# Performance work log

Measured on AMD Instinct MI355X. Metric: run time of the kernel, lower is better.

## Reference

```python
import jax, jax.numpy as jnp
import numpy as np

N, E, FE, H, G, L, OUT = 50000, 300000, 64, 256, 256, 4, 128
BN_EPS = 1e-5


def setup_inputs() -> dict:
    key = jax.random.key(0)
    ks = jax.random.split(key, 12)
    s = 0.05
    return dict(
        x=jax.random.normal(ks[0], (N, H), jnp.float32),
        edge_index=jax.random.randint(ks[1], (2, E), 0, N, dtype=jnp.int64),
        edge_attr=jax.random.normal(ks[2], (E, FE), jnp.float32),
        batch=jnp.sort(jax.random.randint(ks[3], (N,), 0, G, dtype=jnp.int64)),
        bond_W1=jax.random.normal(ks[4], (L, FE, H), jnp.float32) * s,
        bond_b1=jnp.zeros((L, H), jnp.float32),
        bond_W2=jax.random.normal(ks[5], (L, H, H), jnp.float32) * s,
        bond_b2=jnp.zeros((L, H), jnp.float32),
        mlp_W1=jax.random.normal(ks[6], (L, H, H), jnp.float32) * s,
        mlp_b1=jnp.zeros((L, H), jnp.float32),
        mlp_W2=jax.random.normal(ks[7], (L, H, H), jnp.float32) * s,
        mlp_b2=jnp.zeros((L, H), jnp.float32),
        eps=jnp.zeros((L,), jnp.float32),
        bn_gamma=jnp.ones((L, H), jnp.float32),
        bn_beta=jnp.zeros((L, H), jnp.float32),
        fc1_W=jax.random.normal(ks[8], (L * H, H), jnp.float32) * s,
        fc1_b=jnp.zeros((H,), jnp.float32),
        fc4_W=jax.random.normal(ks[9], (H, OUT), jnp.float32) * s,
        fc4_b=jnp.zeros((OUT,), jnp.float32),
    )


def reference(x, edge_index, edge_attr, batch,
              bond_W1, bond_b1, bond_W2, bond_b2,
              mlp_W1, mlp_b1, mlp_W2, mlp_b2,
              eps, bn_gamma, bn_beta,
              fc1_W, fc1_b, fc4_W, fc4_b):
    src, dst = edge_index[0], edge_index[1]  # x_j gathered from src, scatter-add to dst
    x_lst = []
    for l in range(L):
        # bond encoder: Linear -> ReLU -> Linear on edge features [E, FE] -> [E, H]
        e = jax.nn.relu(edge_attr @ bond_W1[l] + bond_b1[l]) @ bond_W2[l] + bond_b2[l]
        # message = relu(x_j + e), aggregate = scatter-add over destination nodes
        msg = jax.nn.relu(x[src] + e)  # [E, H]
        aggr = jax.ops.segment_sum(msg, dst, num_segments=N)  # [N, H]
        h = (1.0 + eps[l]) * x + aggr
        h = jax.nn.relu(h @ mlp_W1[l] + mlp_b1[l]) @ mlp_W2[l] + mlp_b2[l]
        h = jax.nn.relu(h)
        # BatchNorm over the node dimension (training-style batch statistics)
        mu = jnp.mean(h, axis=0)
        var = jnp.var(h, axis=0)
        x = (h - mu) * jax.lax.rsqrt(var + BN_EPS) * bn_gamma[l] + bn_beta[l]
        x_lst.append(x)
    xc = jnp.concatenate(x_lst, axis=-1)  # [N, L*H]
    # global mean pool over graphs
    sums = jax.ops.segment_sum(xc, batch, num_segments=G)  # [G, L*H]
    cnts = jax.ops.segment_sum(jnp.ones((N,), xc.dtype), batch, num_segments=G)
    pooled = sums / jnp.maximum(cnts, 1.0)[:, None]
    h = jax.nn.relu(pooled @ fc1_W + fc1_b)
    # dropout p=0.5 in eval mode -> identity
    return h @ fc4_W + fc4_b  # [G, OUT]
```

## Files before the change

kernel.cpp:

```cpp
#include <hip/hip_runtime.h>

#define NN 50000
#define NE 300000
#define FEA 64
#define HD 256
#define NG 256
#define NL 4
#define OD 128
#define SCB ((NN + 255) / 256)

typedef unsigned short u16;
typedef unsigned int u32;
typedef __attribute__((ext_vector_type(8))) short short8;
typedef __attribute__((ext_vector_type(4))) float f32x4;

__device__ __forceinline__ u16 f2h(float f) {
    union { _Float16 h; u16 u; } v; v.h = (_Float16)f; return v.u;
}
__device__ __forceinline__ float h2f(u16 u) {
    union { u16 u; _Float16 h; } v; v.u = u; return (float)v.h;
}

typedef const __attribute__((address_space(1))) unsigned int gas_u32;
typedef __attribute__((address_space(3))) unsigned int las_u32;
__device__ __forceinline__ void gld16(const void* g, void* l) {
    __builtin_amdgcn_global_load_lds((gas_u32*)g, (las_u32*)l, 16, 0, 0);
}

__global__ __launch_bounds__(256, 2) void edge_k(
    const u16* __restrict__ eattrS, const u16* __restrict__ W1t,
    const float* __restrict__ bb1, const u16* __restrict__ W2t,
    const float* __restrict__ bb2,
    const int* __restrict__ srcI, const int* __restrict__ dstI,
    const u16* __restrict__ xh, float* __restrict__ aggr)
{
    __shared__ __align__(16) u16 bufW[256 * 64];
    __shared__ __align__(16) u16 bufT[64 * 256];
    __shared__ int dstL[64];
    __shared__ int srcL[64];
    const int tid = threadIdx.x;
    const int lane = tid & 63;
    const int w = tid >> 6;
    const int q = lane >> 4, c15 = lane & 15;
    const int e0 = blockIdx.x * 64;
    const int wb = tid & ~63;

    if (tid < 64) {
        int er = e0 + tid;
        int erc = er < NE ? er : NE - 1;
        dstL[tid] = (er < NE) ? dstI[erc] : -1;
        srcL[tid] = srcI[erc];
    }
#pragma unroll
    for (int it = 0; it < 2; ++it) {
        const int i = it * 256 + tid;
        const int m = i >> 3, kb = i & 7;
        int row = e0 + m; if (row > NE - 1) row = NE - 1;
        gld16(eattrS + (size_t)row * FEA + ((kb ^ (m & 7)) * 8),
              &bufT[(it * 256 + wb) * 8]);
    }
#pragma unroll
    for (int it = 0; it < 8; ++it) {
        const int i = it * 256 + tid;
        const int n = i >> 3, kb = i & 7;
        gld16(W1t + (size_t)n * FEA + ((kb ^ (n & 7)) * 8),
              &bufW[(it * 256 + wb) * 8]);
    }
    __syncthreads();

    f32x4 acc1[4][4];
#pragma unroll
    for (int i = 0; i < 4; ++i)
#pragma unroll
        for (int j = 0; j < 4; ++j) acc1[i][j] = (f32x4)0.0f;
#pragma unroll
    for (int s = 0; s < 2; ++s) {
        short8 af[4], bf[4];
#pragma unroll
        for (int t = 0; t < 4; ++t) {
            const int kga = s * 4 + q;
            const int mm = t * 16 + c15;
            af[t] = *(const short8*)&bufT[mm * 64 + ((kga ^ (mm & 7)) * 8)];
            const int nn = w * 64 + t * 16 + c15;
            bf[t] = *(const short8*)&bufW[nn * 64 + ((kga ^ (nn & 7)) * 8)];
        }
        __builtin_amdgcn_s_setprio(1);
#pragma unroll
        for (int tm = 0; tm < 4; ++tm)
#pragma unroll
            for (int tn = 0; tn < 4; ++tn)
                acc1[tm][tn] = __builtin_amdgcn_mfma_f32_16x16x32_f16(
                    af[tm], bf[tn], acc1[tm][tn], 0, 0, 0);
        __builtin_amdgcn_s_setprio(0);
    }
    __syncthreads();

    auto stageW2 = [&](int cc) {
        const int k0c = cc * 32;
        const int hB = (cc & 1) * 1024;
#pragma unroll
        for (int it = 0; it < 4; ++it) {
            const int i = it * 256 + tid;
            const int n = i >> 2, j = i & 3;
            gld16(W2t + (size_t)n * HD + k0c + ((j ^ ((n >> 1) & 3)) * 8),
                  &bufW[(hB + it * 256 + wb) * 8]);
        }
    };
    stageW2(0);

    {
        float b1f[4];
#pragma unroll
        for (int tn = 0; tn < 4; ++tn)
            b1f[tn] = bb1[w * 64 + tn * 16 + c15];
#pragma unroll
        for (int tm = 0; tm < 4; ++tm)
#pragma unroll
            for (int tn = 0; tn < 4; ++tn) {
                const int col = w * 64 + tn * 16 + c15;
                const int kb = col >> 3;
#pragma unroll
                for (int r = 0; r < 4; ++r) {
                    const int row = tm * 16 + q * 4 + r;
                    float v = acc1[tm][tn][r] + b1f[tn];
                    v = v > 0.0f ? v : 0.0f;
                    bufT[row * 256 + ((kb ^ (row & 7)) * 8) + (col & 7)] = f2h(v);
                }
            }
    }
    __syncthreads();

    f32x4 acc2[4][4];
#pragma unroll
    for (int i = 0; i < 4; ++i)
#pragma unroll
        for (int j = 0; j < 4; ++j) acc2[i][j] = (f32x4)0.0f;
#pragma unroll
    for (int c = 0; c < 8; ++c) {
        if (c < 7) {
            stageW2(c + 1);
        } else {
#pragma unroll
            for (int it = 0; it < 4; ++it) {
                const int i = it * 256 + tid;
                const int row = i >> 5, ch = i & 31;
                gld16(xh + (size_t)srcL[row] * HD + ch * 8,
                      &bufW[(it * 256 + wb) * 8]);
            }
        }
        short8 af[4], bf[4];
        const u16* hp = &bufW[(c & 1) * 8192];
#pragma unroll
        for (int t = 0; t < 4; ++t) {
            const int mm = t * 16 + c15;
            const int kbg = c * 4 + q;
            af[t] = *(const short8*)&bufT[mm * 256 + ((kbg ^ (mm & 7)) * 8)];
            const int nn = w * 64 + t * 16 + c15;
            bf[t] = *(const short8*)&hp[nn * 32 + ((q ^ ((nn >> 1) & 3)) * 8)];
        }
        __builtin_amdgcn_s_setprio(1);
#pragma unroll
        for (int tm = 0; tm < 4; ++tm)
#pragma unroll
            for (int tn = 0; tn < 4; ++tn)
                acc2[tm][tn] = __builtin_amdgcn_mfma_f32_16x16x32_f16(
                    af[tm], bf[tn], acc2[tm][tn], 0, 0, 0);
        __builtin_amdgcn_s_setprio(0);
        __syncthreads();
    }

#pragma unroll
    for (int it = 0; it < 4; ++it) {
        const int i = 1024 + it * 256 + tid;
        const int row = i >> 5, ch = i & 31;
        gld16(xh + (size_t)srcL[row] * HD + ch * 8,
              &bufW[(1024 + it * 256 + wb) * 8]);
    }
    float b2f[4];
#pragma unroll
    for (int tn = 0; tn < 4; ++tn)
        b2f[tn] = bb2[w * 64 + tn * 16 + c15];
    __syncthreads();

#pragma unroll
    for (int tm = 0; tm < 4; ++tm)
#pragma unroll
        for (int r = 0; r < 4; ++r) {
            const int row = tm * 16 + q * 4 + r;
            if (e0 + row < NE) {
#pragma unroll
                for (int tn = 0; tn < 4; ++tn) {
                    const int col = w * 64 + tn * 16 + c15;
                    float v = acc2[tm][tn][r] + b2f[tn]
                            + h2f(bufW[row * 256 + col]);
                    v = v > 0.0f ? v : 0.0f;
                    bufT[row * 256 + col] = f2h(v);
                }
            }
        }
    __syncthreads();

    {
        const int hiR = (NE - e0 < 64) ? (NE - e0) : 64;
        float s = 0.0f;
        int cur = dstL[0];
        for (int rI = 0; rI < hiR; ++rI) {
            const int d = dstL[rI];
            if (d != cur) {
                if (s != 0.0f) unsafeAtomicAdd(&aggr[(size_t)cur * HD + tid], s);
                cur = d; s = 0.0f;
            }
            s += h2f(bufT[rI * 256 + tid]);
        }
        if (cur >= 0 && s != 0.0f)
            unsafeAtomicAdd(&aggr[(size_t)cur * HD + tid], s);
    }
}

__global__ __launch_bounds__(256, 2) void node_k(
    const u16* __restrict__ xh, const float* __restrict__ aggr,
    const float* __restrict__ epsv, int l,
    const u16* __restrict__ M1t, const float* __restrict__ mb1,
    const u16* __restrict__ M2t, const float* __restrict__ mb2,
    u16* __restrict__ hb, float* __restrict__ bns, float* __restrict__ bnq)
{
    __shared__ __align__(16) u16 bufW[256 * 64];
    __shared__ __align__(16) u16 bufT[64 * 256];
    const int tid = threadIdx.x;
    const int lane = tid & 63;
    const int w = tid >> 6;
    const int q = lane >> 4, c15 = lane & 15;
    const int n0b = blockIdx.x * 64;
    const float e1 = 1.0f + epsv[l];
    const int wb = tid & ~63;

    auto stageM = [&](const u16* Mt, int cc) {
        const int k0c = cc * 32;
        const int hB = (cc & 1) * 1024;
#pragma unroll
        for (int it = 0; it < 4; ++it) {
            const int i = it * 256 + tid;
            const int n = i >> 2, j = i & 3;
            gld16(Mt + (size_t)n * HD + k0c + ((j ^ ((n >> 1) & 3)) * 8),
                  &bufW[(hB + it * 256 + wb) * 8]);
        }
    };
    stageM(M1t, 0);

#pragma unroll
    for (int it = 0; it < 8; ++it) {
        const int i = it * 256 + tid;
        const int m = i >> 5, kb = i & 31;
        int row = n0b + m; if (row > NN - 1) row = NN - 1;
        const size_t base = (size_t)row * HD + kb * 8;
        short8 xv = *(const short8*)(xh + base);
        float4 a0 = *(const float4*)(aggr + base);
        float4 a1 = *(const float4*)(aggr + base + 4);
        u16 o[8];
        o[0] = f2h(e1 * h2f((u16)xv[0]) + a0.x);
        o[1] = f2h(e1 * h2f((u16)xv[1]) + a0.y);
        o[2] = f2h(e1 * h2f((u16)xv[2]) + a0.z);
        o[3] = f2h(e1 * h2f((u16)xv[3]) + a0.w);
        o[4] = f2h(e1 * h2f((u16)xv[4]) + a1.x);
        o[5] = f2h(e1 * h2f((u16)xv[5]) + a1.y);
        o[6] = f2h(e1 * h2f((u16)xv[6]) + a1.z);
        o[7] = f2h(e1 * h2f((u16)xv[7]) + a1.w);
        *(short8*)&bufT[m * 256 + ((kb ^ (m & 7)) * 8)] = *(short8*)o;
    }
    __syncthreads();

    f32x4 acc1[4][4];
#pragma unroll
    for (int i = 0; i < 4; ++i)
#pragma unroll
        for (int j = 0; j < 4; ++j) acc1[i][j] = (f32x4)0.0f;
#pragma unroll
    for (int c = 0; c < 8; ++c) {
        if (c < 7) stageM(M1t, c + 1);
        else       stageM(M2t, 0);
        short8 af[4], bf[4];
        const u16* hp = &bufW[(c & 1) * 8192];
#pragma unroll
        for (int t = 0; t < 4; ++t) {
            const int mm = t * 16 + c15;
            const int kbg = c * 4 + q;
            af[t] = *(const short8*)&bufT[mm * 256 + ((kbg ^ (mm & 7)) * 8)];
            const int nn = w * 64 + t * 16 + c15;
            bf[t] = *(const short8*)&hp[nn * 32 + ((q ^ ((nn >> 1) & 3)) * 8)];
        }
        __builtin_amdgcn_s_setprio(1);
#pragma unroll
        for (int tm = 0; tm < 4; ++tm)
#pragma unroll
            for (int tn = 0; tn < 4; ++tn)
                acc1[tm][tn] = __builtin_amdgcn_mfma_f32_16x16x32_f16(
                    af[tm], bf[tn], acc1[tm][tn], 0, 0, 0);
        __builtin_amdgcn_s_setprio(0);
        __syncthreads();
    }

    {
        float b1f[4];
#pragma unroll
        for (int tn = 0; tn < 4; ++tn)
            b1f[tn] = mb1[w * 64 + tn * 16 + c15];
#pragma unroll
        for (int tm = 0; tm < 4; ++tm)
#pragma unroll
            for (int tn = 0; tn < 4; ++tn) {
                const int col = w * 64 + tn * 16 + c15;
                const int kb = col >> 3;
#pragma unroll
                for (int r = 0; r < 4; ++r) {
                    const int row = tm * 16 + q * 4 + r;
                    float v = acc1[tm][tn][r] + b1f[tn];
                    v = v > 0.0f ? v : 0.0f;
                    bufT[row * 256 + ((kb ^ (row & 7)) * 8) + (col & 7)] = f2h(v);
                }
            }
    }
    __syncthreads();

    f32x4 acc2[4][4];
#pragma unroll
    for (int i = 0; i < 4; ++i)
#pragma unroll
        for (int j = 0; j < 4; ++j) acc2[i][j] = (f32x4)0.0f;
#pragma unroll
    for (int c = 0; c < 8; ++c) {
        if (c < 7) stageM(M2t, c + 1);
        short8 af[4], bf[4];
        const u16* hp = &bufW[(c & 1) * 8192];
#pragma unroll
        for (int t = 0; t < 4; ++t) {
            const int mm = t * 16 + c15;
            const int kbg = c * 4 + q;
            af[t] = *(const short8*)&bufT[mm * 256 + ((kbg ^ (mm & 7)) * 8)];
            const int nn = w * 64 + t * 16 + c15;
            bf[t] = *(const short8*)&hp[nn * 32 + ((q ^ ((nn >> 1) & 3)) * 8)];
        }
        __builtin_amdgcn_s_setprio(1);
#pragma unroll
        for (int tm = 0; tm < 4; ++tm)
#pragma unroll
            for (int tn = 0; tn < 4; ++tn)
                acc2[tm][tn] = __builtin_amdgcn_mfma_f32_16x16x32_f16(
                    af[tm], bf[tn], acc2[tm][tn], 0, 0, 0);
        __builtin_amdgcn_s_setprio(0);
        __syncthreads();
    }

    float b2f[4];
#pragma unroll
    for (int tn = 0; tn < 4; ++tn)
        b2f[tn] = mb2[w * 64 + tn * 16 + c15];
    float ps[4] = {0, 0, 0, 0}, pq[4] = {0, 0, 0, 0};
#pragma unroll
    for (int tm = 0; tm < 4; ++tm) {
#pragma unroll
        for (int r = 0; r < 4; ++r) {
            const int grow = n0b + tm * 16 + q * 4 + r;
            if (grow < NN) {
#pragma unroll
                for (int tn = 0; tn < 4; ++tn) {
                    const int col = w * 64 + tn * 16 + c15;
                    float v = acc2[tm][tn][r] + b2f[tn];
                    v = v > 0.0f ? v : 0.0f;
                    hb[(size_t)grow * HD + col] = f2h(v);
                    ps[tn] += v; pq[tn] += v * v;
                }
            }
        }
    }
#pragma unroll
    for (int tn = 0; tn < 4; ++tn) {
        float s = ps[tn], sq = pq[tn];
        s += __shfl_down(s, 32, 64);  sq += __shfl_down(sq, 32, 64);
        s += __shfl_down(s, 16, 64);  sq += __shfl_down(sq, 16, 64);
        if (q == 0) {
            const int col = w * 64 + tn * 16 + c15;
            unsafeAtomicAdd(&bns[col], s);
            unsafeAtomicAdd(&bnq[col], sq);
        }
    }
}


__global__ void transpose_k(const float* __restrict__ in, u16* __restrict__ oh,
                            int Kw, int Nw) {
    int i = blockIdx.x * blockDim.x + threadIdx.x;
    int tot = NL * Kw * Nw;
    if (i < tot) {
        int l = i / (Kw * Nw), rem = i % (Kw * Nw);
        int k = rem / Nw, n = rem % Nw;
        oh[(size_t)l * Kw * Nw + (size_t)n * Kw + k] = f2h(in[i]);
    }
}

__global__ void cvt_k(const float* __restrict__ in, u16* __restrict__ outh, int tot) {
    int i = blockIdx.x * blockDim.x + threadIdx.x;
    if (i < tot) outh[i] = f2h(in[i]);
}

__global__ void egather_k(const float* __restrict__ eattr, const int* __restrict__ perm,
                          u16* __restrict__ eattrS) {
    int i = blockIdx.x * blockDim.x + threadIdx.x;
    if (i < NE * FEA) {
        int row = i >> 6, k = i & 63;
        eattrS[i] = f2h(eattr[(size_t)perm[row] * FEA + k]);
    }
}

__global__ void zero_layer_k(float* __restrict__ aggr, float* __restrict__ bns,
                             float* __restrict__ bnq) {
    int i = blockIdx.x * blockDim.x + threadIdx.x;
    if (i < NN * HD) aggr[i] = 0.0f;
    if (i < HD) { bns[i] = 0.0f; bnq[i] = 0.0f; }
}

__global__ void zerof_k(float* __restrict__ p, int n) {
    int i = blockIdx.x * blockDim.x + threadIdx.x;
    if (i < n) p[i] = 0.0f;
}

__global__ void bnfin_k(const float* __restrict__ bns, const float* __restrict__ bnq,
                        const float* __restrict__ gamma, const float* __restrict__ beta,
                        int l, float* __restrict__ ab) {
    int c = threadIdx.x;
    float mu = bns[c] * (1.0f / (float)NN);
    float var = bnq[c] * (1.0f / (float)NN) - mu * mu;
    if (var < 0.0f) var = 0.0f;
    float a = gamma[l * HD + c] * rsqrtf(var + 1e-5f);
    float b = beta[l * HD + c] - mu * a;
    ab[c] = a; ab[HD + c] = b;
}

__global__ void bnapply_k(const u16* __restrict__ hb, const float* __restrict__ ab,
                          const int* __restrict__ batch, u16* __restrict__ xh,
                          float* __restrict__ pooled, int l) {
    const int t = threadIdx.x;
    const int n0 = blockIdx.x * 64;
    const float a = ab[t], b = ab[HD + t];
    const int hi = (NN - n0 < 64) ? (NN - n0) : 64;
    float s = 0.0f;
    int cur = batch[n0];
    for (int r = 0; r < hi; ++r) {
        const size_t idx = (size_t)(n0 + r) * HD + t;
        float v = a * h2f(hb[idx]) + b;
        xh[idx] = f2h(v);
        const int g = batch[n0 + r];
        if (g != cur) {
            unsafeAtomicAdd(&pooled[(size_t)cur * (NL * HD) + l * HD + t], s);
            s = 0.0f; cur = g;
        }
        s += v;
    }
    unsafeAtomicAdd(&pooled[(size_t)cur * (NL * HD) + l * HD + t], s);
}


__global__ void zeroi_k(int* __restrict__ a, int n) {
    int i = blockIdx.x * blockDim.x + threadIdx.x;
    if (i < n) a[i] = 0;
}

__global__ void hist_k(const int* __restrict__ dst, int* __restrict__ hist) {
    int e = blockIdx.x * blockDim.x + threadIdx.x;
    if (e < NE) atomicAdd(&hist[dst[e]], 1);
}

__global__ void sumblk_k(const int* __restrict__ hist, int* __restrict__ psum) {
    __shared__ int red[256];
    int b = blockIdx.x, t = threadIdx.x, i = b * 256 + t;
    red[t] = (i < NN) ? hist[i] : 0;
    __syncthreads();
    for (int o = 128; o > 0; o >>= 1) {
        if (t < o) red[t] += red[t + o];
        __syncthreads();
    }
    if (t == 0) psum[b] = red[0];
}

__global__ void scanblk_k(int* __restrict__ psum) {
    __shared__ int sc[256];
    int t = threadIdx.x;
    int v = (t < SCB) ? psum[t] : 0;
    sc[t] = v; __syncthreads();
    for (int o = 1; o < 256; o <<= 1) {
        int x = (t >= o) ? sc[t - o] : 0;
        __syncthreads(); sc[t] += x; __syncthreads();
    }
    if (t < SCB) psum[t] = sc[t] - v;
}

__global__ void scanfin_k(const int* __restrict__ hist, const int* __restrict__ psum,
                          int* __restrict__ rowptr) {
    __shared__ int sc[256];
    int b = blockIdx.x, t = threadIdx.x, i = b * 256 + t;
    int v = (i < NN) ? hist[i] : 0;
    sc[t] = v; __syncthreads();
    for (int o = 1; o < 256; o <<= 1) {
        int x = (t >= o) ? sc[t - o] : 0;
        __syncthreads(); sc[t] += x; __syncthreads();
    }
    if (i < NN) rowptr[i] = psum[b] + sc[t] - v;
    if (i == NN - 1) rowptr[NN] = psum[b] + sc[t];
}

__global__ void copyi_k(const int* __restrict__ src, int* __restrict__ dst, int n) {
    int i = blockIdx.x * blockDim.x + threadIdx.x;
    if (i < n) dst[i] = src[i];
}

__global__ void scatter_k(const int* __restrict__ dst, int* __restrict__ next,
                          int* __restrict__ perm) {
    int e = blockIdx.x * blockDim.x + threadIdx.x;
    if (e < NE) {
        int p = atomicAdd(&next[dst[e]], 1);
        perm[p] = e;
    }
}

__global__ void permsd_k(const int* __restrict__ eidx, const int* __restrict__ perm,
                         int* __restrict__ srcS, int* __restrict__ dstS) {
    int i = blockIdx.x * blockDim.x + threadIdx.x;
    if (i < NE) {
        int e = perm[i];
        srcS[i] = eidx[e];
        dstS[i] = eidx[NE + e];
    }
}


__global__ void zcnt_k(int* __restrict__ cnts) {
    if (threadIdx.x < NG) cnts[threadIdx.x] = 0;
}

__global__ void count_k(const int* __restrict__ batch, int* __restrict__ cnts) {
    int i = blockIdx.x * blockDim.x + threadIdx.x;
    if (i < NN) atomicAdd(&cnts[batch[i]], 1);
}

__global__ void fc_k(const float* __restrict__ pooled, const int* __restrict__ cnts,
                     const float* __restrict__ W1, const float* __restrict__ b1,
                     const float* __restrict__ W4, const float* __restrict__ b4,
                     float* __restrict__ out) {
    __shared__ float pl[NL * HD];
    __shared__ float hm[HD];
    int g = blockIdx.x, t = threadIdx.x;
    const float inv = 1.0f / fmaxf((float)cnts[g], 1.0f);
#pragma unroll
    for (int j = 0; j < 4; ++j)
        pl[t + j * 256] = pooled[(size_t)g * 1024 + t + j * 256] * inv;
    __syncthreads();
    float a = b1[t];
    for (int k = 0; k < 1024; ++k) a += pl[k] * W1[k * 256 + t];
    hm[t] = a > 0.0f ? a : 0.0f;
    __syncthreads();
    if (t < OD) {
        float o = b4[t];
        for (int k = 0; k < 256; ++k) o += hm[k] * W4[k * OD + t];
        out[g * OD + t] = o;
    }
}


extern "C" void kernel_launch(void* const* d_in, const int* in_sizes, int n_in,
                              void* d_out, int out_size, void* d_ws, size_t ws_size,
                              hipStream_t stream) {
    const float* x_in  = (const float*)d_in[0];
    const int*   eidx  = (const int*)d_in[1];
    const float* eattr = (const float*)d_in[2];
    const int*   batch = (const int*)d_in[3];
    const float* bW1   = (const float*)d_in[4];
    const float* bb1   = (const float*)d_in[5];
    const float* bW2   = (const float*)d_in[6];
    const float* bb2   = (const float*)d_in[7];
    const float* mW1   = (const float*)d_in[8];
    const float* mb1   = (const float*)d_in[9];
    const float* mW2   = (const float*)d_in[10];
    const float* mb2   = (const float*)d_in[11];
    const float* epsv  = (const float*)d_in[12];
    const float* gamma = (const float*)d_in[13];
    const float* beta  = (const float*)d_in[14];
    const float* fc1W  = (const float*)d_in[15];
    const float* fc1b  = (const float*)d_in[16];
    const float* fc4W  = (const float*)d_in[17];
    const float* fc4b  = (const float*)d_in[18];
    float* out = (float*)d_out;
    (void)in_sizes; (void)n_in; (void)out_size; (void)ws_size;

    size_t off = 0;
    auto alloc = [&](size_t bytes) -> char* {
        char* r = (char*)d_ws + off;
        off = (off + bytes + 255) & ~(size_t)255;
        return r;
    };
    u16*   xh   = (u16*)alloc((size_t)NN * HD * 2);
    float* aggr = (float*)alloc((size_t)NN * HD * 4);
    u16*   hb   = (u16*)alloc((size_t)NN * HD * 2);
    u16*   eattrS = (u16*)alloc((size_t)NE * FEA * 2);
    u16*   W1t  = (u16*)alloc((size_t)NL * FEA * HD * 2);
    u16*   W2t  = (u16*)alloc((size_t)NL * HD * HD * 2);
    u16*   M1t  = (u16*)alloc((size_t)NL * HD * HD * 2);
    u16*   M2t  = (u16*)alloc((size_t)NL * HD * HD * 2);
    float* bns  = (float*)alloc(HD * 4);
    float* bnq  = (float*)alloc(HD * 4);
    float* ab   = (float*)alloc(2 * HD * 4);
    int*   cnts = (int*)alloc(NG * 4);
    float* pooled = (float*)alloc((size_t)NG * NL * HD * 4);
    int*   hist  = (int*)alloc((size_t)NN * 4);
    int*   psum  = (int*)alloc((size_t)SCB * 4);
    int*   rowptr = (int*)alloc((size_t)(NN + 1) * 4);
    int*   perm  = (int*)alloc((size_t)NE * 4);
    int*   srcS  = (int*)alloc((size_t)NE * 4);
    int*   dstS  = (int*)alloc((size_t)NE * 4);

    const int NEL = NN * HD;
    const int EB = (NEL + 255) / 256;
    const int NEB = (NE + 255) / 256;

    transpose_k<<<(NL * FEA * HD + 255) / 256, 256, 0, stream>>>(bW1, W1t, FEA, HD);
    transpose_k<<<(NL * HD * HD + 255) / 256, 256, 0, stream>>>(bW2, W2t, HD, HD);
    transpose_k<<<(NL * HD * HD + 255) / 256, 256, 0, stream>>>(mW1, M1t, HD, HD);
    transpose_k<<<(NL * HD * HD + 255) / 256, 256, 0, stream>>>(mW2, M2t, HD, HD);

    cvt_k<<<EB, 256, 0, stream>>>(x_in, xh, NEL);

    zeroi_k<<<(NN + 255) / 256, 256, 0, stream>>>(hist, NN);
    hist_k<<<NEB, 256, 0, stream>>>(eidx + NE, hist);
    sumblk_k<<<SCB, 256, 0, stream>>>(hist, psum);
    scanblk_k<<<1, 256, 0, stream>>>(psum);
    scanfin_k<<<SCB, 256, 0, stream>>>(hist, psum, rowptr);
    copyi_k<<<(NN + 255) / 256, 256, 0, stream>>>(rowptr, hist, NN);
    scatter_k<<<NEB, 256, 0, stream>>>(eidx + NE, hist, perm);
    permsd_k<<<NEB, 256, 0, stream>>>(eidx, perm, srcS, dstS);
    egather_k<<<(NE * FEA + 255) / 256, 256, 0, stream>>>(eattr, perm, eattrS);

    zcnt_k<<<1, 256, 0, stream>>>(cnts);
    count_k<<<(NN + 255) / 256, 256, 0, stream>>>(batch, cnts);
    zerof_k<<<(NG * NL * HD + 255) / 256, 256, 0, stream>>>(pooled, NG * NL * HD);

    const int EGB = (NE + 63) / 64;
    const int NGB = (NN + 63) / 64;

    for (int l = 0; l < NL; ++l) {
        zero_layer_k<<<EB, 256, 0, stream>>>(aggr, bns, bnq);
        edge_k<<<EGB, 256, 0, stream>>>(
            eattrS, W1t + (size_t)l * FEA * HD, bb1 + l * HD,
            W2t + (size_t)l * HD * HD, bb2 + l * HD,
            srcS, dstS, xh, aggr);
        node_k<<<NGB, 256, 0, stream>>>(
            xh, aggr, epsv, l,
            M1t + (size_t)l * HD * HD, mb1 + l * HD,
            M2t + (size_t)l * HD * HD, mb2 + l * HD,
            hb, bns, bnq);
        bnfin_k<<<1, HD, 0, stream>>>(bns, bnq, gamma, beta, l, ab);
        bnapply_k<<<NGB, 256, 0, stream>>>(hb, ab, batch, xh, pooled, l);
    }
    fc_k<<<NG, 256, 0, stream>>>(pooled, cnts, fc1W, fc1b, fc4W, fc4b, out);
}
```

Baseline: 1.342 ms.

## Transpose MFMA outputs for vectorized LDS stores and column-wise segment reduction

Swaps the MFMA A/B operands in the first GEMM of the edge and node kernels so each lane holds four consecutive output features. The bias-ReLU epilogue can then write 8-byte packed fp16 vectors into the swizzled LDS tile instead of scalar 2-byte stores. The edge kernel's final message tile is stored transposed, so the scatter-add loop reads 16-byte vectors per feature column rather than one fp16 per row. Destination indices are now read directly from global memory inside the reduction loop instead of being staged in shared memory, which adds repeated scalar global loads of dstI.

```diff
diff --git a/kernel.cpp b/kernel.cpp
--- a/kernel.cpp
+++ b/kernel.cpp
@@ -12,6 +12,7 @@
 typedef unsigned short u16;
 typedef unsigned int u32;
 typedef __attribute__((ext_vector_type(8))) short short8;
+typedef __attribute__((ext_vector_type(4))) short s16x4;
 typedef __attribute__((ext_vector_type(4))) float f32x4;
 
 __device__ __forceinline__ u16 f2h(float f) {
@@ -36,7 +37,6 @@
 {
     __shared__ __align__(16) u16 bufW[256 * 64];
     __shared__ __align__(16) u16 bufT[64 * 256];
-    __shared__ int dstL[64];
     __shared__ int srcL[64];
     const int tid = threadIdx.x;
     const int lane = tid & 63;
@@ -48,7 +48,6 @@
     if (tid < 64) {
         int er = e0 + tid;
         int erc = er < NE ? er : NE - 1;
-        dstL[tid] = (er < NE) ? dstI[erc] : -1;
         srcL[tid] = srcI[erc];
     }
 #pragma unroll
@@ -90,7 +89,7 @@
 #pragma unroll
             for (int tn = 0; tn < 4; ++tn)
                 acc1[tm][tn] = __builtin_amdgcn_mfma_f32_16x16x32_f16(
-                    af[tm], bf[tn], acc1[tm][tn], 0, 0, 0);
+                    bf[tm], af[tn], acc1[tm][tn], 0, 0, 0);
         __builtin_amdgcn_s_setprio(0);
     }
     __syncthreads();
@@ -109,24 +108,24 @@
     stageW2(0);
 
     {
-        float b1f[4];
-#pragma unroll
-        for (int tn = 0; tn < 4; ++tn)
-            b1f[tn] = bb1[w * 64 + tn * 16 + c15];
-#pragma unroll
-        for (int tm = 0; tm < 4; ++tm)
+#pragma unroll
+        for (int tm = 0; tm < 4; ++tm) {
+            const float4 b1v = *(const float4*)(bb1 + w * 64 + tm * 16 + q * 4);
+            const int kb = w * 8 + tm * 2 + (q >> 1);
 #pragma unroll
             for (int tn = 0; tn < 4; ++tn) {
-                const int col = w * 64 + tn * 16 + c15;
-                const int kb = col >> 3;
+                const int edge = tn * 16 + c15;
+                s16x4 o;
 #pragma unroll
                 for (int r = 0; r < 4; ++r) {
-                    const int row = tm * 16 + q * 4 + r;
-                    float v = acc1[tm][tn][r] + b1f[tn];
+                    float v = acc1[tm][tn][r] + ((const float*)&b1v)[r];
                     v = v > 0.0f ? v : 0.0f;
-                    bufT[row * 256 + ((kb ^ (row & 7)) * 8) + (col & 7)] = f2h(v);
+                    o[r] = (short)f2h(v);
                 }
+                *(s16x4*)((char*)bufT + edge * 512 +
+                          ((kb ^ (edge & 7)) << 4) + ((q & 1) << 3)) = o;
             }
+        }
     }
     __syncthreads();
 
@@ -183,34 +182,44 @@
     __syncthreads();
 
 #pragma unroll
-    for (int tm = 0; tm < 4; ++tm)
-#pragma unroll
-        for (int r = 0; r < 4; ++r) {
-            const int row = tm * 16 + q * 4 + r;
-            if (e0 + row < NE) {
-#pragma unroll
-                for (int tn = 0; tn < 4; ++tn) {
-                    const int col = w * 64 + tn * 16 + c15;
-                    float v = acc2[tm][tn][r] + b2f[tn]
-                            + h2f(bufW[row * 256 + col]);
-                    v = v > 0.0f ? v : 0.0f;
-                    bufT[row * 256 + col] = f2h(v);
+    for (int tm = 0; tm < 4; ++tm) {
+        const int rc = tm * 2 + (q >> 1);
+#pragma unroll
+        for (int tn = 0; tn < 4; ++tn) {
+            const int col = w * 64 + tn * 16 + c15;
+            s16x4 o;
+#pragma unroll
+            for (int r = 0; r < 4; ++r) {
+                const int row = tm * 16 + q * 4 + r;
+                float v = acc2[tm][tn][r] + b2f[tn]
+                        + h2f(bufW[row * 256 + col]);
+                v = v > 0.0f ? v : 0.0f;
+                o[r] = (short)f2h(v);
+            }
+            *(s16x4*)((char*)bufT + col * 128 +
+                      ((rc ^ (col & 7)) << 4) + ((q & 1) << 3)) = o;
+        }
+    }
+    __syncthreads();
+
+    {
+        const char* bT = (const char*)bufT;
+        float s = 0.0f;
+        int cur = dstI[e0];
+#pragma unroll
+        for (int j = 0; j < 8; ++j) {
+            short8 m8 = *(const short8*)(bT + tid * 128 + ((j ^ (tid & 7)) << 4));
+#pragma unroll
+            for (int si = 0; si < 8; ++si) {
+                const int er = e0 + j * 8 + si;
+                const int d = (er < NE) ? dstI[er] : -1;
+                if (d != cur) {
+                    if (cur >= 0 && s != 0.0f)
+                        unsafeAtomicAdd(&aggr[(size_t)cur * HD + tid], s);
+                    cur = d; s = 0.0f;
                 }
+                s += h2f((u16)m8[si]);
             }
-        }
-    __syncthreads();
-
-    {
-        const int hiR = (NE - e0 < 64) ? (NE - e0) : 64;
-        float s = 0.0f;
-        int cur = dstL[0];
-        for (int rI = 0; rI < hiR; ++rI) {
-            const int d = dstL[rI];
-            if (d != cur) {
-                if (s != 0.0f) unsafeAtomicAdd(&aggr[(size_t)cur * HD + tid], s);
-                cur = d; s = 0.0f;
-            }
-            s += h2f(bufT[rI * 256 + tid]);
         }
         if (cur >= 0 && s != 0.0f)
             unsafeAtomicAdd(&aggr[(size_t)cur * HD + tid], s);
@@ -294,30 +303,30 @@
 #pragma unroll
             for (int tn = 0; tn < 4; ++tn)
                 acc1[tm][tn] = __builtin_amdgcn_mfma_f32_16x16x32_f16(
-                    af[tm], bf[tn], acc1[tm][tn], 0, 0, 0);
+                    bf[tm], af[tn], acc1[tm][tn], 0, 0, 0);
         __builtin_amdgcn_s_setprio(0);
         __syncthreads();
     }
 
     {
-        float b1f[4];
-#pragma unroll
-        for (int tn = 0; tn < 4; ++tn)
-            b1f[tn] = mb1[w * 64 + tn * 16 + c15];
-#pragma unroll
-        for (int tm = 0; tm < 4; ++tm)
+#pragma unroll
+        for (int tm = 0; tm < 4; ++tm) {
+            const float4 b1v = *(const float4*)(mb1 + w * 64 + tm * 16 + q * 4);
+            const int kb = w * 8 + tm * 2 + (q >> 1);
 #pragma unroll
             for (int tn = 0; tn < 4; ++tn) {
-                const int col = w * 64 + tn * 16 + c15;
-                const int kb = col >> 3;
+                const int node = tn * 16 + c15;
+                s16x4 o;
 #pragma unroll
                 for (int r = 0; r < 4; ++r) {
-                    const int row = tm * 16 + q * 4 + r;
-                    float v = acc1[tm][tn][r] + b1f[tn];
+                    float v = acc1[tm][tn][r] + ((const float*)&b1v)[r];
                     v = v > 0.0f ? v : 0.0f;
-                    bufT[row * 256 + ((kb ^ (row & 7)) * 8) + (col & 7)] = f2h(v);
+                    o[r] = (short)f2h(v);
                 }
+                *(s16x4*)((char*)bufT + node * 512 +
+                          ((kb ^ (node & 7)) << 4) + ((q & 1) << 3)) = o;
             }
+        }
     }
     __syncthreads();
 
```

Result: faster. 1.268 ms (-5.5%).
